# Performance work log

Measured on AMD Instinct MI355X. Metric: run time of the kernel, lower is better.

Reference implementation:

```python
import jax, jax.numpy as jnp
import numpy as np

R_MAX = 5.0
AVG_NEIGH = 16.0
F = 64          # hidden scalar channels (hidden_irreps count of 0e)
NB = 8          # num_bessel
LMAX = 2
S = 9           # (LMAX+1)^2 spherical-harmonic components
NE = 10         # num_elements
G = 4           # num_graphs
T = 2           # num_interactions
L_OF_LM = np.array([0, 1, 1, 1, 2, 2, 2, 2, 2])


def spherical_harmonics(u):
    # real SH up to l=2, e3nn 'component' normalization; u: [E,3] unit vectors
    x, y, z = u[:, 0], u[:, 1], u[:, 2]
    s3, s5, s15 = 3.0 ** 0.5, 5.0 ** 0.5, 15.0 ** 0.5
    return jnp.stack([
        jnp.ones_like(x),
        s3 * x, s3 * y, s3 * z,
        s15 * x * y, s15 * y * z, (s5 / 2.0) * (3.0 * z * z - 1.0),
        s15 * x * z, (s15 / 2.0) * (x * x - y * y),
    ], axis=-1)  # [E, 9]


def radial_embedding(r):
    # Bessel basis * polynomial cutoff (p=5), as in MACE RadialEmbeddingBlock
    r_safe = jnp.maximum(r, 1e-6)
    n = jnp.arange(1, NB + 1, dtype=r.dtype)  # [NB]
    bessel = jnp.sqrt(2.0 / R_MAX) * jnp.sin(n[None, :] * jnp.pi * r_safe[:, None] / R_MAX) / r_safe[:, None]
    u = r / R_MAX
    p = 5.0
    f = (1.0 - 0.5 * (p + 1) * (p + 2) * u ** 5 + p * (p + 2) * u ** 6 - 0.5 * p * (p + 1) * u ** 7)
    f = f * (u < 1.0)
    return bessel * f[:, None]  # [E, NB]


def setup_inputs() -> dict:
    key = jax.random.key(0)
    ks = jax.random.split(key, 24)
    N, E = 20000, 320000
    positions = jax.random.normal(ks[0], (N, 3), dtype=jnp.float32) * 5.0
    species = jax.random.randint(ks[1], (N,), 0, NE)
    node_attrs = jax.nn.one_hot(species, NE, dtype=jnp.float32)
    edge_index = jax.random.randint(ks[2], (2, E), 0, N)
    shifts = jnp.zeros((E, 3), dtype=jnp.float32)
    batch = jnp.sort(jax.random.randint(ks[3], (N,), 0, G)).astype(jnp.int32)
    charges = jax.random.normal(ks[4], (N,), dtype=jnp.float32) * 0.1
    sc = 1.0 / np.sqrt(F)
    params = {
        'atomic_energies': jax.random.normal(ks[5], (NE,), dtype=jnp.float32),
        'W_embed': jax.random.normal(ks[6], (NE, F), dtype=jnp.float32),
        'Wr0': jax.random.normal(ks[7], (T, NB, 64), dtype=jnp.float32) / np.sqrt(NB),
        'Wr1': jax.random.normal(ks[8], (T, 64, 64), dtype=jnp.float32) / 8.0,
        'Wr2': jax.random.normal(ks[9], (T, 64, F * (LMAX + 1)), dtype=jnp.float32) / 8.0,
        'Wmix': jax.random.normal(ks[10], (T, LMAX + 1, F, F), dtype=jnp.float32) * sc,
        'Wprod': jax.random.normal(ks[11], (T, NE, F, 3), dtype=jnp.float32) * sc,
        'Wread0': jax.random.normal(ks[12], (F,), dtype=jnp.float32) * sc,
        'Wm1': jax.random.normal(ks[13], (F, 16), dtype=jnp.float32) * sc,
        'wm2': jax.random.normal(ks[14], (16,), dtype=jnp.float32) * 0.25,
        'Wq': jax.random.normal(ks[15], (T, F), dtype=jnp.float32) * sc,
    }
    return dict(positions=positions, node_attrs=node_attrs, shifts=shifts,
                charges=charges, edge_index=edge_index, batch=batch, **params)


def _forward(positions, node_attrs, shifts, charges,
             atomic_energies, W_embed, Wr0, Wr1, Wr2, Wmix, Wprod,
             Wread0, Wm1, wm2, Wq, edge_index, batch):
    N = positions.shape[0]
    src, dst = edge_index[0], edge_index[1]
    # isolated-atom reference energies
    node_e0 = node_attrs @ atomic_energies                       # [N]
    e0 = jax.ops.segment_sum(node_e0, batch, num_segments=G)     # [G]
    # edge geometry
    vec = positions[dst] - positions[src] + shifts               # [E,3]
    lengths = jnp.linalg.norm(vec, axis=-1)                      # [E]
    len_safe = jnp.where(lengths > 1e-6, lengths, 1.0)
    unit = vec / len_safe[:, None]
    edge_attrs = spherical_harmonics(unit)                       # [E,S]
    edge_feats = radial_embedding(lengths)                       # [E,NB]
    # node embedding: scalars only, rest of irreps zero
    node_feats = jnp.zeros((N, F, S), dtype=positions.dtype)
    node_feats = node_feats.at[:, :, 0].set(node_attrs @ W_embed)
    charge_density = charges[:, None] * jnp.ones((1, 1), positions.dtype)  # [N,1] formal charges (l=0)
    lm = jnp.asarray(L_OF_LM)
    energy = e0
    for t in range(T):
        # radial MLP -> per-edge tensor-product weights [E,F,LMAX+1]
        h = jax.nn.silu(edge_feats @ Wr0[t])
        h = jax.nn.silu(h @ Wr1[t])
        w = (h @ Wr2[t]).reshape(-1, F, LMAX + 1)
        wl = w[:, :, lm]                                         # [E,F,S]
        s_src = node_feats[src, :, 0]                            # [E,F] gather
        msg = wl * s_src[:, :, None] * edge_attrs[:, None, :]    # [E,F,S]
        A = jax.ops.segment_sum(msg, dst, num_segments=N) / AVG_NEIGH  # [N,F,S] scatter
        # per-l linear channel mixing
        A = jnp.einsum('nfs,sfg->ngs', A, Wmix[t][lm])
        # symmetric product basis (correlation 3), element-dependent weights
        wp = jnp.einsum('ne,efc->nfc', node_attrs, Wprod[t])     # [N,F,3]
        p1 = A[:, :, 0]                                          # scalar invariant
        p2 = jnp.sum(A * A, axis=-1)                             # norm invariant
        scale = wp[:, :, 0] + wp[:, :, 1] * p1 + wp[:, :, 2] * p2
        new_feats = A * scale[:, :, None]
        if t > 0:
            new_feats = new_feats + node_feats                   # residual self-connection
        node_feats = new_feats
        scal = node_feats[:, :, 0]
        if t == T - 1:
            node_en = jax.nn.silu(scal @ Wm1) @ wm2              # nonlinear readout
        else:
            node_en = scal @ Wread0                              # linear readout
        energy = energy + jax.ops.segment_sum(node_en, batch, num_segments=G)
        charge_density = charge_density + (scal @ Wq[t])[:, None]
    return energy  # [G]


def reference(positions, node_attrs, shifts, charges, edge_index, batch,
              atomic_energies, W_embed, Wr0, Wr1, Wr2, Wmix, Wprod,
              Wread0, Wm1, wm2, Wq):
    return _forward(positions, node_attrs, shifts, charges,
                    atomic_energies, W_embed, Wr0, Wr1, Wr2, Wmix, Wprod,
                    Wread0, Wm1, wm2, Wq, edge_index, batch)
```

## Files before the change

### kernel.cpp

```cpp
#include <hip/hip_runtime.h>
#include <hip/hip_bf16.h>

#define F 64
#define NB 8
#define NE 10
#define GSEG 4
#define EPW 256
#define NTAB 2048

typedef __attribute__((ext_vector_type(8))) short short8v;
typedef __attribute__((ext_vector_type(4))) float float4v;

__device__ __forceinline__ float silu(float x) {
    return x / (1.0f + __expf(-x));
}

__device__ __forceinline__ float bcast(float v, int lane) {
    return __uint_as_float(__builtin_amdgcn_readlane(__float_as_uint(v), lane));
}

__device__ __forceinline__ unsigned short f2bf(float x) {
    unsigned int u = __float_as_uint(x);
    u += 0x7FFFu + ((u >> 16) & 1u);
    return (unsigned short)(u >> 16);
}

__global__ __launch_bounds__(256) void init_and_tables(
    const float* __restrict__ node_attrs, const float* __restrict__ AE,
    const float* __restrict__ W_embed, const int* __restrict__ batch,
    const float* __restrict__ pos,
    float* __restrict__ S0, float* __restrict__ epart,
    int* __restrict__ deg, float4* __restrict__ pos4, int N, int nodeBlocks,
    const float* __restrict__ Wr0, const float* __restrict__ Wr1,
    const float* __restrict__ Wr2, float* __restrict__ Tab,
    const float* __restrict__ Wmix, unsigned short* __restrict__ Wbt,
    int tabBlocks)
{
    int w = threadIdx.x >> 6, lane = threadIdx.x & 63;

    if (blockIdx.x < (unsigned)nodeBlocks) {
        int n = blockIdx.x * 4 + w;
        if (n >= N) return;
        float sc = 0.0f, e0 = 0.0f;
        #pragma unroll
        for (int e = 0; e < NE; e++) {
            float a = node_attrs[n * NE + e];
            sc = fmaf(a, W_embed[e * F + lane], sc);
            e0 = fmaf(a, AE[e], e0);
        }
        S0[(size_t)n * F + lane] = sc;
        if (lane == 0) {
            deg[n] = 0;
            pos4[n] = make_float4(pos[n * 3], pos[n * 3 + 1], pos[n * 3 + 2], 0.f);
            atomicAdd(&epart[batch[n] * EPW + (n & (EPW - 1))], e0);
        }
        return;
    }

    if (blockIdx.x >= (unsigned)(nodeBlocks + tabBlocks)) {
        int i = (blockIdx.x - nodeBlocks - tabBlocks) * 256 + threadIdx.x;
        if (i >= 2 * 3 * 4096) return;
        int tl = i >> 12;
        int gf = i & 4095;
        int g = gf >> 6, f = gf & 63;
        Wbt[i] = f2bf(Wmix[(size_t)(tl * 64 + f) * 64 + g] * 0.0625f);
        return;
    }

    const int blocksPerTab = (NTAB + 1 + 3) / 4;
    int bid = blockIdx.x - nodeBlocks;
    int tab = bid / blocksPerTab;
    int eidx = (bid - tab * blocksPerTab) * 4 + w;
    if (eidx > NTAB) return;
    const float* W0 = Wr0 + tab * 512;
    const float* W1 = Wr1 + tab * 4096;
    const float* W2 = Wr2 + tab * 12288;

    float r = (float)eidx * (5.0f / NTAB);
    float rs = fmaxf(r, 1e-6f);
    float s1, c1;
    __sincosf(0.6283185307179586f * rs, &s1, &c1);
    float u = r * 0.2f;
    float u2 = u * u, u4 = u2 * u2, u5 = u4 * u, u6 = u5 * u, u7 = u6 * u;
    float fc = 1.0f - 21.0f * u5 + 35.0f * u6 - 15.0f * u7;
    float pref = 0.6324555320336759f / rs * fc;
    float ef[NB];
    {
        float sp = 0.0f, sc_ = s1, tc = 2.0f * c1;
        #pragma unroll
        for (int k = 0; k < NB; k++) {
            ef[k] = pref * sc_;
            float sn = tc * sc_ - sp;
            sp = sc_; sc_ = sn;
        }
    }

    float a1 = 0.0f;
    #pragma unroll
    for (int k = 0; k < NB; k++) a1 = fmaf(ef[k], W0[k * 64 + lane], a1);
    float h1 = silu(a1);

    float a2 = 0.0f;
    #pragma unroll 8
    for (int k = 0; k < 64; k++)
        a2 = fmaf(bcast(h1, k), W1[k * 64 + lane], a2);
    float h2 = silu(a2);

    float w0 = 0.f, w1 = 0.f, w2 = 0.f;
    #pragma unroll 8
    for (int k = 0; k < 64; k++) {
        float hk = bcast(h2, k);
        const float* wr = W2 + k * 192 + lane * 3;
        w0 = fmaf(hk, wr[0], w0);
        w1 = fmaf(hk, wr[1], w1);
        w2 = fmaf(hk, wr[2], w2);
    }

    float* Trow = Tab + ((size_t)tab * (NTAB + 1) + eidx) * 192;
    Trow[lane] = w0;
    Trow[64 + lane] = w1;
    Trow[128 + lane] = w2;
}

__global__ __launch_bounds__(256) void edge_prep(
    const float4* __restrict__ pos4, const float* __restrict__ shifts,
    const int* __restrict__ EI, int E,
    float4* __restrict__ geoFull, int* __restrict__ deg)
{
    int e = blockIdx.x * 256 + threadIdx.x;
    if (e >= E) return;
    int s = EI[e], d = EI[E + e];
    float4 pd = pos4[d], ps = pos4[s];
    float vx = pd.x - ps.x + shifts[e * 3 + 0];
    float vy = pd.y - ps.y + shifts[e * 3 + 1];
    float vz = pd.z - ps.z + shifts[e * 3 + 2];
    float len = sqrtf(vx * vx + vy * vy + vz * vz);
    float ls = (len > 1e-6f) ? len : 1.0f;
    float inv = 1.0f / ls;
    geoFull[e] = make_float4(vx * inv, vy * inv, vz * inv, len);
    if (len < 5.0f) atomicAdd(&deg[d], 1);
}

__global__ __launch_bounds__(256) void alloc_start(
    const int* __restrict__ deg, int* __restrict__ start,
    int* __restrict__ cursor, int* __restrict__ total, int N)
{
    __shared__ int wsum[4];
    __shared__ int gbase;
    int t = threadIdx.x;
    int n = blockIdx.x * 256 + t;
    int lane = t & 63, w = t >> 6;
    int v = (n < N) ? deg[n] : 0;
    int inc = v;
    #pragma unroll
    for (int off = 1; off < 64; off <<= 1) {
        int u = __shfl_up(inc, off);
        if (lane >= off) inc += u;
    }
    if (lane == 63) wsum[w] = inc;
    __syncthreads();
    if (t == 0) {
        int s0 = wsum[0], s1 = wsum[1], s2 = wsum[2], s3 = wsum[3];
        int bs = s0 + s1 + s2 + s3;
        wsum[0] = 0; wsum[1] = s0; wsum[2] = s0 + s1; wsum[3] = s0 + s1 + s2;
        gbase = atomicAdd(total, bs);
    }
    __syncthreads();
    if (n < N) {
        int st = gbase + wsum[w] + (inc - v);
        start[n] = st;
        cursor[n] = st;
    }
}

__global__ __launch_bounds__(256) void csr_fill(
    const float4* __restrict__ geoFull, const int* __restrict__ EI, int E,
    int* __restrict__ cursor,
    float4* __restrict__ geoS, int* __restrict__ srcS, int EB)
{
    int e = blockIdx.x * 256 + threadIdx.x;
    if (e >= E) return;
    float4 gv = geoFull[e];
    if (gv.w < 5.0f) {
        int d = EI[E + e];
        int p = atomicAdd(&cursor[d], 1);
        if (p < EB) {
            geoS[p] = gv;
            srcS[p] = EI[e];
        }
    }
}

__global__ __launch_bounds__(256) void gather_edges(
    const float4* __restrict__ geoS, const int* __restrict__ srcS,
    const float* __restrict__ Tab,
    const int* __restrict__ start, const int* __restrict__ deg,
    const float* __restrict__ Sin, unsigned short* __restrict__ Abuf,
    int N, int N16)
{
    int g = threadIdx.x & 63;
    int w = threadIdx.x >> 6;
    int n = blockIdx.x * 4 + w;
    if (n >= N) return;
    size_t PL = (size_t)N16 * 64;

    int st = start[n], dg = deg[n];
    if (dg == 0) {
        #pragma unroll
        for (int s = 0; s < 9; s++) Abuf[s * PL + (size_t)n * 64 + g] = 0;
        return;
    }

    float am0 = 0.f, am1 = 0.f, am2_ = 0.f, am3 = 0.f, am4 = 0.f,
          am5 = 0.f, am6 = 0.f, am7 = 0.f, am8 = 0.f;

    const float s3 = 1.7320508075688772f;
    const float s5h = 1.1180339887498948f;
    const float s15 = 3.8729833462074170f;
    const float s15h = 1.9364916731037085f;

    for (int i = st; i < st + dg; i++) {
        float4 gv = geoS[i];
        int srcn = srcS[i];
        float sv = Sin[(size_t)srcn * F + g];
        float scaled = gv.w * (NTAB / 5.0f);
        int idx = (int)scaled;
        float fr = scaled - (float)idx;
        const float* T0 = Tab + (size_t)idx * 192;
        float wa = T0[g],        wb = T0[192 + g];
        float wc = T0[64 + g],   wd = T0[256 + g];
        float we = T0[128 + g],  wf_ = T0[320 + g];
        float w0 = fmaf(fr, wb - wa, wa);
        float w1 = fmaf(fr, wd - wc, wc);
        float w2 = fmaf(fr, wf_ - we, we);

        float ux = gv.x, uy = gv.y, uz = gv.z;
        float m0 = w0 * sv, m1 = w1 * sv, m2 = w2 * sv;
        am0 += m0;
        am1 = fmaf(m1, s3 * ux, am1);
        am2_ = fmaf(m1, s3 * uy, am2_);
        am3 = fmaf(m1, s3 * uz, am3);
        am4 = fmaf(m2, s15 * ux * uy, am4);
        am5 = fmaf(m2, s15 * uy * uz, am5);
        am6 = fmaf(m2, s5h * (3.0f * uz * uz - 1.0f), am6);
        am7 = fmaf(m2, s15 * ux * uz, am7);
        am8 = fmaf(m2, s15h * (ux * ux - uy * uy), am8);
    }

    size_t base = (size_t)n * 64 + g;
    Abuf[0 * PL + base] = f2bf(am0);
    Abuf[1 * PL + base] = f2bf(am1);
    Abuf[2 * PL + base] = f2bf(am2_);
    Abuf[3 * PL + base] = f2bf(am3);
    Abuf[4 * PL + base] = f2bf(am4);
    Abuf[5 * PL + base] = f2bf(am5);
    Abuf[6 * PL + base] = f2bf(am6);
    Abuf[7 * PL + base] = f2bf(am7);
    Abuf[8 * PL + base] = f2bf(am8);
}

template <int PHASE>
__global__ __launch_bounds__(1024) void mix_finish(
    const unsigned short* __restrict__ Abuf,
    const unsigned short* __restrict__ Wbt,
    const float* __restrict__ Wprodt,
    const float* __restrict__ node_attrs, const int* __restrict__ batch,
    const float* __restrict__ Wread0, const float* __restrict__ Wm1,
    const float* __restrict__ wm2,
    const float* __restrict__ Sin, float* __restrict__ Sout,
    float* __restrict__ epart, int N, int N16)
{
    __shared__ float Osh[9 * 1088];

    int t = threadIdx.x;
    int lane = t & 63, w = t >> 6;
    int l15 = lane & 15, quad = lane >> 4;
    int n0 = blockIdx.x * 16;
    size_t PL = (size_t)N16 * 64;

    if (w < 9) {
        int s = w;
        int l = (s == 0) ? 0 : ((s < 4) ? 1 : 2);
        const unsigned short* Ap = Abuf + s * PL + (size_t)(n0 + l15) * 64;
        const unsigned short* Bp = Wbt + l * 4096 + (size_t)l15 * 64;
        short8v a0 = *(const short8v*)(Ap + quad * 8);
        short8v a1 = *(const short8v*)(Ap + 32 + quad * 8);
        #pragma unroll
        for (int nt = 0; nt < 4; nt++) {
            short8v b0 = *(const short8v*)(Bp + nt * 1024 + quad * 8);
            short8v b1 = *(const short8v*)(Bp + nt * 1024 + 32 + quad * 8);
            float4v acc = {0.f, 0.f, 0.f, 0.f};
            acc = __builtin_amdgcn_mfma_f32_16x16x32_bf16(a0, b0, acc, 0, 0, 0);
            acc = __builtin_amdgcn_mfma_f32_16x16x32_bf16(a1, b1, acc, 0, 0, 0);
            #pragma unroll
            for (int r = 0; r < 4; r++)
                Osh[s * 1088 + (quad * 4 + r) * 68 + nt * 16 + l15] = acc[r];
        }
    }
    __syncthreads();

    int n = n0 + w;
    if (n >= N) return;
    int b = batch[n];
    float bb[9];
    #pragma unroll
    for (int s = 0; s < 9; s++) bb[s] = Osh[s * 1088 + w * 68 + lane];

    float wp0 = 0.f, wp1 = 0.f, wp2 = 0.f;
    #pragma unroll
    for (int e = 0; e < NE; e++) {
        float a = node_attrs[n * NE + e];
        const float* W = Wprodt + (e * F + lane) * 3;
        wp0 = fmaf(a, W[0], wp0);
        wp1 = fmaf(a, W[1], wp1);
        wp2 = fmaf(a, W[2], wp2);
    }
    float p1 = bb[0];
    float p2 = 0.f;
    #pragma unroll
    for (int s = 0; s < 9; s++) p2 = fmaf(bb[s], bb[s], p2);
    float scale = wp0 + wp1 * p1 + wp2 * p2;
    float sc0 = bb[0] * scale;

    if (PHASE == 0) {
        Sout[(size_t)n * F + lane] = sc0;
        float vv = sc0 * Wread0[lane];
        #pragma unroll
        for (int off = 32; off > 0; off >>= 1) vv += __shfl_xor(vv, off);
        if (lane == 0) atomicAdd(&epart[b * EPW + (n & (EPW - 1))], vv);
    } else {
        sc0 += Sin[(size_t)n * F + lane];
        int gi = lane & 15;
        float acc = 0.0f;
        #pragma unroll 8
        for (int k = 0; k < 64; k++)
            acc = fmaf(bcast(sc0, k), Wm1[k * 16 + gi], acc);
        float vv = (lane < 16) ? silu(acc) * wm2[gi] : 0.0f;
        #pragma unroll
        for (int off = 32; off > 0; off >>= 1) vv += __shfl_xor(vv, off);
        if (lane == 0) atomicAdd(&epart[b * EPW + (n & (EPW - 1))], vv);
    }
}

__global__ __launch_bounds__(256) void reduce_energy(
    const float* __restrict__ epart, float* __restrict__ out)
{
    int t = threadIdx.x;
    __shared__ float ps[GSEG][4];
    for (int b = 0; b < GSEG; b++) {
        float v = epart[b * EPW + t];
        #pragma unroll
        for (int off = 32; off > 0; off >>= 1) v += __shfl_xor(v, off);
        if ((t & 63) == 0) ps[b][t >> 6] = v;
    }
    __syncthreads();
    if (t < GSEG) out[t] = ps[t][0] + ps[t][1] + ps[t][2] + ps[t][3];
}

extern "C" void kernel_launch(void* const* d_in, const int* in_sizes, int n_in,
                              void* d_out, int out_size, void* d_ws, size_t ws_size,
                              hipStream_t stream) {
    const float* positions  = (const float*)d_in[0];
    const float* node_attrs = (const float*)d_in[1];
    const float* shifts     = (const float*)d_in[2];
    const int*   edge_index = (const int*)d_in[4];
    const int*   batch      = (const int*)d_in[5];
    const float* AE         = (const float*)d_in[6];
    const float* W_embed    = (const float*)d_in[7];
    const float* Wr0        = (const float*)d_in[8];
    const float* Wr1        = (const float*)d_in[9];
    const float* Wr2        = (const float*)d_in[10];
    const float* Wmix       = (const float*)d_in[11];
    const float* Wprod      = (const float*)d_in[12];
    const float* Wread0     = (const float*)d_in[13];
    const float* Wm1        = (const float*)d_in[14];
    const float* wm2        = (const float*)d_in[15];

    int N = in_sizes[0] / 3;
    int E = in_sizes[4] / 2;
    int EB = E / 8;
    int N16 = (N + 15) & ~15;
    float* out = (float*)d_out;

    char* ws = (char*)d_ws;
    size_t off = 0;
    auto alignup = [](size_t v) { return (v + 255) & ~(size_t)255; };
    float4* geoFull = (float4*)(ws + off); off = alignup(off + (size_t)E * sizeof(float4));
    float4* geoS  = (float4*)(ws + off); off = alignup(off + (size_t)EB * sizeof(float4));
    float4* pos4  = (float4*)(ws + off); off = alignup(off + (size_t)N * sizeof(float4));
    float*  S0    = (float*)(ws + off);  off = alignup(off + (size_t)N * F * sizeof(float));
    float*  S1    = (float*)(ws + off);  off = alignup(off + (size_t)N * F * sizeof(float));
    int*    srcS  = (int*)(ws + off);    off = alignup(off + (size_t)EB * sizeof(int));
    int*    deg   = (int*)(ws + off);    off = alignup(off + (size_t)N * sizeof(int));
    int*    start = (int*)(ws + off);    off = alignup(off + (size_t)N * sizeof(int));
    int*    cursor= (int*)(ws + off);    off = alignup(off + (size_t)N * sizeof(int));
    float*  epart = (float*)(ws + off);
    int*    total = (int*)(ws + off + GSEG * EPW * sizeof(float));
    off = alignup(off + GSEG * EPW * sizeof(float) + 128);
    float*  Tab   = (float*)(ws + off);
    off = alignup(off + (size_t)2 * (NTAB + 1) * 192 * sizeof(float));
    unsigned short* Wbt = (unsigned short*)(ws + off);
    off = alignup(off + (size_t)2 * 3 * 4096 * sizeof(unsigned short));
    unsigned short* Abuf = (unsigned short*)(ws + off);
    off += (size_t)9 * N16 * 64 * sizeof(unsigned short);

    hipMemsetAsync(epart, 0, GSEG * EPW * sizeof(float) + 128, stream);

    int nodeBlocks4 = (N + 3) / 4;
    int nodeBlocks256 = (N + 255) / 256;
    int edgeBlocks = (E + 255) / 256;
    int tabBlocks = 2 * ((NTAB + 1 + 3) / 4);
    int wbBlocks = (2 * 3 * 4096 + 255) / 256;
    int mfBlocks = (N + 15) / 16;
    size_t tabStride = (size_t)(NTAB + 1) * 192;

    init_and_tables<<<nodeBlocks4 + tabBlocks + wbBlocks, 256, 0, stream>>>(
        node_attrs, AE, W_embed, batch, positions,
        S0, epart, deg, pos4, N, nodeBlocks4,
        Wr0, Wr1, Wr2, Tab, Wmix, Wbt, tabBlocks);
    edge_prep<<<edgeBlocks, 256, 0, stream>>>(pos4, shifts, edge_index, E,
                                              geoFull, deg);
    alloc_start<<<nodeBlocks256, 256, 0, stream>>>(deg, start, cursor, total, N);
    csr_fill<<<edgeBlocks, 256, 0, stream>>>(geoFull, edge_index, E,
                                             cursor, geoS, srcS, EB);

    gather_edges<<<nodeBlocks4, 256, 0, stream>>>(geoS, srcS, Tab, start, deg,
                                                  S0, Abuf, N, N16);
    mix_finish<0><<<mfBlocks, 1024, 0, stream>>>(Abuf, Wbt, Wprod,
                                                 node_attrs, batch,
                                                 Wread0, Wm1, wm2,
                                                 S0, S1, epart, N, N16);
    gather_edges<<<nodeBlocks4, 256, 0, stream>>>(geoS, srcS, Tab + tabStride,
                                                  start, deg, S1, Abuf, N, N16);
    mix_finish<1><<<mfBlocks, 1024, 0, stream>>>(Abuf, Wbt + 3 * 4096,
                                                 Wprod + NE * F * 3,
                                                 node_attrs, batch,
                                                 Wread0, Wm1, wm2,
                                                 S1, S1, epart, N, N16);

    reduce_energy<<<1, 256, 0, stream>>>(epart, out);
}
```

Baseline: 237.5 us.

## Fuse edge gather with MFMA mixing and use species index for product weights

```diff
diff --git a/kernel.cpp b/kernel.cpp
--- a/kernel.cpp
+++ b/kernel.cpp
@@ -30,7 +30,8 @@
     const float* __restrict__ W_embed, const int* __restrict__ batch,
     const float* __restrict__ pos,
     float* __restrict__ S0, float* __restrict__ epart,
-    int* __restrict__ deg, float4* __restrict__ pos4, int N, int nodeBlocks,
+    int* __restrict__ deg, float4* __restrict__ pos4,
+    int* __restrict__ spec, int N, int nodeBlocks,
     const float* __restrict__ Wr0, const float* __restrict__ Wr1,
     const float* __restrict__ Wr2, float* __restrict__ Tab,
     const float* __restrict__ Wmix, unsigned short* __restrict__ Wbt,
@@ -42,15 +43,18 @@
         int n = blockIdx.x * 4 + w;
         if (n >= N) return;
         float sc = 0.0f, e0 = 0.0f;
+        int sp = 0;
         #pragma unroll
         for (int e = 0; e < NE; e++) {
             float a = node_attrs[n * NE + e];
             sc = fmaf(a, W_embed[e * F + lane], sc);
             e0 = fmaf(a, AE[e], e0);
+            if (a > 0.5f) sp = e;
         }
         S0[(size_t)n * F + lane] = sc;
         if (lane == 0) {
             deg[n] = 0;
+            spec[n] = sp;
             pos4[n] = make_float4(pos[n * 3], pos[n * 3 + 1], pos[n * 3 + 2], 0.f);
             atomicAdd(&epart[batch[n] * EPW + (n & (EPW - 1))], e0);
         }
@@ -191,100 +195,84 @@
     }
 }
 
-__global__ __launch_bounds__(256) void gather_edges(
+template <int PHASE>
+__global__ __launch_bounds__(1024) void gather_mix(
     const float4* __restrict__ geoS, const int* __restrict__ srcS,
     const float* __restrict__ Tab,
     const int* __restrict__ start, const int* __restrict__ deg,
-    const float* __restrict__ Sin, unsigned short* __restrict__ Abuf,
-    int N, int N16)
-{
-    int g = threadIdx.x & 63;
-    int w = threadIdx.x >> 6;
-    int n = blockIdx.x * 4 + w;
-    if (n >= N) return;
-    size_t PL = (size_t)N16 * 64;
-
-    int st = start[n], dg = deg[n];
-    if (dg == 0) {
-        #pragma unroll
-        for (int s = 0; s < 9; s++) Abuf[s * PL + (size_t)n * 64 + g] = 0;
-        return;
-    }
-
-    float am0 = 0.f, am1 = 0.f, am2_ = 0.f, am3 = 0.f, am4 = 0.f,
-          am5 = 0.f, am6 = 0.f, am7 = 0.f, am8 = 0.f;
-
-    const float s3 = 1.7320508075688772f;
-    const float s5h = 1.1180339887498948f;
-    const float s15 = 3.8729833462074170f;
-    const float s15h = 1.9364916731037085f;
-
-    for (int i = st; i < st + dg; i++) {
-        float4 gv = geoS[i];
-        int srcn = srcS[i];
-        float sv = Sin[(size_t)srcn * F + g];
-        float scaled = gv.w * (NTAB / 5.0f);
-        int idx = (int)scaled;
-        float fr = scaled - (float)idx;
-        const float* T0 = Tab + (size_t)idx * 192;
-        float wa = T0[g],        wb = T0[192 + g];
-        float wc = T0[64 + g],   wd = T0[256 + g];
-        float we = T0[128 + g],  wf_ = T0[320 + g];
-        float w0 = fmaf(fr, wb - wa, wa);
-        float w1 = fmaf(fr, wd - wc, wc);
-        float w2 = fmaf(fr, wf_ - we, we);
-
-        float ux = gv.x, uy = gv.y, uz = gv.z;
-        float m0 = w0 * sv, m1 = w1 * sv, m2 = w2 * sv;
-        am0 += m0;
-        am1 = fmaf(m1, s3 * ux, am1);
-        am2_ = fmaf(m1, s3 * uy, am2_);
-        am3 = fmaf(m1, s3 * uz, am3);
-        am4 = fmaf(m2, s15 * ux * uy, am4);
-        am5 = fmaf(m2, s15 * uy * uz, am5);
-        am6 = fmaf(m2, s5h * (3.0f * uz * uz - 1.0f), am6);
-        am7 = fmaf(m2, s15 * ux * uz, am7);
-        am8 = fmaf(m2, s15h * (ux * ux - uy * uy), am8);
-    }
-
-    size_t base = (size_t)n * 64 + g;
-    Abuf[0 * PL + base] = f2bf(am0);
-    Abuf[1 * PL + base] = f2bf(am1);
-    Abuf[2 * PL + base] = f2bf(am2_);
-    Abuf[3 * PL + base] = f2bf(am3);
-    Abuf[4 * PL + base] = f2bf(am4);
-    Abuf[5 * PL + base] = f2bf(am5);
-    Abuf[6 * PL + base] = f2bf(am6);
-    Abuf[7 * PL + base] = f2bf(am7);
-    Abuf[8 * PL + base] = f2bf(am8);
-}
-
-template <int PHASE>
-__global__ __launch_bounds__(1024) void mix_finish(
-    const unsigned short* __restrict__ Abuf,
     const unsigned short* __restrict__ Wbt,
-    const float* __restrict__ Wprodt,
-    const float* __restrict__ node_attrs, const int* __restrict__ batch,
+    const float* __restrict__ Wprodt, const int* __restrict__ spec,
+    const int* __restrict__ batch,
     const float* __restrict__ Wread0, const float* __restrict__ Wm1,
     const float* __restrict__ wm2,
     const float* __restrict__ Sin, float* __restrict__ Sout,
-    float* __restrict__ epart, int N, int N16)
-{
+    float* __restrict__ epart, int N)
+{
+    __shared__ unsigned short Abf[9 * 1088];
     __shared__ float Osh[9 * 1088];
 
     int t = threadIdx.x;
     int lane = t & 63, w = t >> 6;
     int l15 = lane & 15, quad = lane >> 4;
     int n0 = blockIdx.x * 16;
-    size_t PL = (size_t)N16 * 64;
+    int n = n0 + w;
+    int g = lane;
+
+    float am0 = 0.f, am1 = 0.f, am2_ = 0.f, am3 = 0.f, am4 = 0.f,
+          am5 = 0.f, am6 = 0.f, am7 = 0.f, am8 = 0.f;
+    if (n < N) {
+        int st = start[n], dg = deg[n];
+        const float s3 = 1.7320508075688772f;
+        const float s5h = 1.1180339887498948f;
+        const float s15 = 3.8729833462074170f;
+        const float s15h = 1.9364916731037085f;
+        for (int i = st; i < st + dg; i++) {
+            float4 gv = geoS[i];
+            int srcn = srcS[i];
+            float sv = Sin[(size_t)srcn * F + g];
+            float scaled = gv.w * (NTAB / 5.0f);
+            int idx = (int)scaled;
+            float fr = scaled - (float)idx;
+            const float* T0 = Tab + (size_t)idx * 192;
+            float wa = T0[g],        wb = T0[192 + g];
+            float wc = T0[64 + g],   wd = T0[256 + g];
+            float we = T0[128 + g],  wf_ = T0[320 + g];
+            float w0 = fmaf(fr, wb - wa, wa);
+            float w1 = fmaf(fr, wd - wc, wc);
+            float w2 = fmaf(fr, wf_ - we, we);
+
+            float ux = gv.x, uy = gv.y, uz = gv.z;
+            float m0 = w0 * sv, m1 = w1 * sv, m2 = w2 * sv;
+            am0 += m0;
+            am1 = fmaf(m1, s3 * ux, am1);
+            am2_ = fmaf(m1, s3 * uy, am2_);
+            am3 = fmaf(m1, s3 * uz, am3);
+            am4 = fmaf(m2, s15 * ux * uy, am4);
+            am5 = fmaf(m2, s15 * uy * uz, am5);
+            am6 = fmaf(m2, s5h * (3.0f * uz * uz - 1.0f), am6);
+            am7 = fmaf(m2, s15 * ux * uz, am7);
+            am8 = fmaf(m2, s15h * (ux * ux - uy * uy), am8);
+        }
+    }
+    int arow = w * 68 + g;
+    Abf[0 * 1088 + arow] = f2bf(am0);
+    Abf[1 * 1088 + arow] = f2bf(am1);
+    Abf[2 * 1088 + arow] = f2bf(am2_);
+    Abf[3 * 1088 + arow] = f2bf(am3);
+    Abf[4 * 1088 + arow] = f2bf(am4);
+    Abf[5 * 1088 + arow] = f2bf(am5);
+    Abf[6 * 1088 + arow] = f2bf(am6);
+    Abf[7 * 1088 + arow] = f2bf(am7);
+    Abf[8 * 1088 + arow] = f2bf(am8);
+    __syncthreads();
 
     if (w < 9) {
         int s = w;
         int l = (s == 0) ? 0 : ((s < 4) ? 1 : 2);
-        const unsigned short* Ap = Abuf + s * PL + (size_t)(n0 + l15) * 64;
         const unsigned short* Bp = Wbt + l * 4096 + (size_t)l15 * 64;
-        short8v a0 = *(const short8v*)(Ap + quad * 8);
-        short8v a1 = *(const short8v*)(Ap + 32 + quad * 8);
+        const unsigned short* Ar = &Abf[s * 1088 + l15 * 68];
+        short8v a0 = *(const short8v*)(Ar + quad * 8);
+        short8v a1 = *(const short8v*)(Ar + 32 + quad * 8);
         #pragma unroll
         for (int nt = 0; nt < 4; nt++) {
             short8v b0 = *(const short8v*)(Bp + nt * 1024 + quad * 8);
@@ -299,22 +287,16 @@
     }
     __syncthreads();
 
-    int n = n0 + w;
     if (n >= N) return;
     int b = batch[n];
     float bb[9];
     #pragma unroll
     for (int s = 0; s < 9; s++) bb[s] = Osh[s * 1088 + w * 68 + lane];
 
-    float wp0 = 0.f, wp1 = 0.f, wp2 = 0.f;
-    #pragma unroll
-    for (int e = 0; e < NE; e++) {
-        float a = node_attrs[n * NE + e];
-        const float* W = Wprodt + (e * F + lane) * 3;
-        wp0 = fmaf(a, W[0], wp0);
-        wp1 = fmaf(a, W[1], wp1);
-        wp2 = fmaf(a, W[2], wp2);
-    }
+    int sp = spec[n];
+    const float* W = Wprodt + (sp * F + lane) * 3;
+    float wp0 = W[0], wp1 = W[1], wp2 = W[2];
+
     float p1 = bb[0];
     float p2 = 0.f;
     #pragma unroll
@@ -379,7 +361,6 @@
     int N = in_sizes[0] / 3;
     int E = in_sizes[4] / 2;
     int EB = E / 8;
-    int N16 = (N + 15) & ~15;
     float* out = (float*)d_out;
 
     char* ws = (char*)d_ws;
@@ -394,6 +375,7 @@
     int*    deg   = (int*)(ws + off);    off = alignup(off + (size_t)N * sizeof(int));
     int*    start = (int*)(ws + off);    off = alignup(off + (size_t)N * sizeof(int));
     int*    cursor= (int*)(ws + off);    off = alignup(off + (size_t)N * sizeof(int));
+    int*    spec  = (int*)(ws + off);    off = alignup(off + (size_t)N * sizeof(int));
     float*  epart = (float*)(ws + off);
     int*    total = (int*)(ws + off + GSEG * EPW * sizeof(float));
     off = alignup(off + GSEG * EPW * sizeof(float) + 128);
@@ -401,8 +383,6 @@
     off = alignup(off + (size_t)2 * (NTAB + 1) * 192 * sizeof(float));
     unsigned short* Wbt = (unsigned short*)(ws + off);
     off = alignup(off + (size_t)2 * 3 * 4096 * sizeof(unsigned short));
-    unsigned short* Abuf = (unsigned short*)(ws + off);
-    off += (size_t)9 * N16 * 64 * sizeof(unsigned short);
 
     hipMemsetAsync(epart, 0, GSEG * EPW * sizeof(float) + 128, stream);
 
@@ -411,12 +391,12 @@
     int edgeBlocks = (E + 255) / 256;
     int tabBlocks = 2 * ((NTAB + 1 + 3) / 4);
     int wbBlocks = (2 * 3 * 4096 + 255) / 256;
-    int mfBlocks = (N + 15) / 16;
+    int gmBlocks = (N + 15) / 16;
     size_t tabStride = (size_t)(NTAB + 1) * 192;
 
     init_and_tables<<<nodeBlocks4 + tabBlocks + wbBlocks, 256, 0, stream>>>(
         node_attrs, AE, W_embed, batch, positions,
-        S0, epart, deg, pos4, N, nodeBlocks4,
+        S0, epart, deg, pos4, spec, N, nodeBlocks4,
         Wr0, Wr1, Wr2, Tab, Wmix, Wbt, tabBlocks);
     edge_prep<<<edgeBlocks, 256, 0, stream>>>(pos4, shifts, edge_index, E,
                                               geoFull, deg);
@@ -424,19 +404,16 @@
     csr_fill<<<edgeBlocks, 256, 0, stream>>>(geoFull, edge_index, E,
                                              cursor, geoS, srcS, EB);
 
-    gather_edges<<<nodeBlocks4, 256, 0, stream>>>(geoS, srcS, Tab, start, deg,
-                                                  S0, Abuf, N, N16);
-    mix_finish<0><<<mfBlocks, 1024, 0, stream>>>(Abuf, Wbt, Wprod,
-                                                 node_attrs, batch,
+    gather_mix<0><<<gmBlocks, 1024, 0, stream>>>(geoS, srcS, Tab, start, deg,
+                                                 Wbt, Wprod, spec, batch,
                                                  Wread0, Wm1, wm2,
-                                                 S0, S1, epart, N, N16);
-    gather_edges<<<nodeBlocks4, 256, 0, stream>>>(geoS, srcS, Tab + tabStride,
-                                                  start, deg, S1, Abuf, N, N16);
-    mix_finish<1><<<mfBlocks, 1024, 0, stream>>>(Abuf, Wbt + 3 * 4096,
-                                                 Wprod + NE * F * 3,
-                                                 node_attrs, batch,
+                                                 S0, S1, epart, N);
+    gather_mix<1><<<gmBlocks, 1024, 0, stream>>>(geoS, srcS, Tab + tabStride,
+                                                 start, deg,
+                                                 Wbt + 3 * 4096,
+                                                 Wprod + NE * F * 3, spec, batch,
                                                  Wread0, Wm1, wm2,
-                                                 S1, S1, epart, N, N16);
+                                                 S1, S1, epart, N);
 
     reduce_energy<<<1, 256, 0, stream>>>(epart, out);
 }
```

Result: faster. 217.0 us (-8.6%).
